# Optimization experiments

Measured on AMD Instinct MI355X. Metric: run time of the kernel, lower is better.

Reference implementation:

```python
import jax, jax.numpy as jnp
import numpy as np

B, N, D, H = 4, 2048, 64, 8

def setup_inputs() -> dict:
    key = jax.random.key(0)
    ks = jax.random.split(key, 6)
    s = 0.05
    return {
        "x":  jax.random.normal(ks[0], (B, N, D), dtype=jnp.float32),
        "Wq": jax.random.normal(ks[1], (D, D * H), dtype=jnp.float32) * s,
        "Wk": jax.random.normal(ks[2], (D, D * H), dtype=jnp.float32) * s,
        "Wv": jax.random.normal(ks[3], (D, D * H), dtype=jnp.float32) * s,
        "Wu": jax.random.normal(ks[4], (D * H, D), dtype=jnp.float32) * s,
        "bu": jnp.zeros((D,), dtype=jnp.float32),
    }

def reference(x, Wq, Wk, Wv, Wu, bu):
    b, n, d = x.shape
    h = Wq.shape[1] // d
    # projections: each head has full width d (per the original module)
    q = (x @ Wq).reshape(b, n, h, d).transpose(0, 2, 1, 3)  # [b,h,n,d]
    k = (x @ Wk).reshape(b, n, h, d).transpose(0, 2, 1, 3)
    v = (x @ Wv).reshape(b, n, h, d).transpose(0, 2, 1, 3)
    scores = jnp.einsum('bhnd,bhmd->bhnm', q, k) / jnp.sqrt(jnp.float32(d))
    w = jax.nn.softmax(scores, axis=-1)
    y = jnp.einsum('bhnm,bhmd->bhnd', w, v)          # [b,h,n,d]
    y = y.transpose(0, 2, 1, 3).reshape(b, n, h * d)  # [b,n,h*d]
    return y @ Wu + bu
```

## Files before the change

kernel.cpp:

```cpp
#include <hip/hip_runtime.h>
#include <hip/hip_bf16.h>

#define BB 4
#define NN 2048
#define DD 64
#define HH 8
#define DHH 512

typedef __bf16 bf16_t;
typedef __bf16 bf16x8 __attribute__((ext_vector_type(8)));
typedef __bf16 bf16x4 __attribute__((ext_vector_type(4)));
typedef float f32x4 __attribute__((ext_vector_type(4)));
typedef long long i64;
typedef i64 i64x2 __attribute__((ext_vector_type(2)));

__device__ __forceinline__ void dma16(const void* g, void* l) {
    __builtin_amdgcn_global_load_lds(
        (const __attribute__((address_space(1))) unsigned int*)g,
        (__attribute__((address_space(3))) unsigned int*)l,
        16, 0, 0);
}

#define MFMA __builtin_amdgcn_mfma_f32_16x16x32_bf16
#define MFMA8 __builtin_amdgcn_mfma_f32_16x16x32_fp8_fp8

#define QSCALE 0.18033688011112042f


__global__ __launch_bounds__(256) void prep(
    const float* __restrict__ Wq, const float* __restrict__ Wk,
    const float* __restrict__ Wv, const float* __restrict__ Wu,
    bf16_t* __restrict__ Wqt, bf16_t* __restrict__ Wkt,
    bf16_t* __restrict__ Wvt, bf16_t* __restrict__ Wut)
{
    const int bid = blockIdx.x, tid = threadIdx.x;
    if (bid < 12) {
        const int m = bid >> 2, slice = bid & 3;
        const float* src = (m == 0) ? Wq : (m == 1) ? Wk : Wv;
        bf16_t* dst = (m == 0) ? Wqt : (m == 1) ? Wkt : Wvt;
        const float scale = (m == 0) ? QSCALE : 1.0f;
        const int dc = slice * 128 + (tid >> 1);
        const int kbase = (tid & 1) * 32;
        #pragma unroll
        for (int k0 = 0; k0 < 4; ++k0) {
            bf16x8 p;
            #pragma unroll
            for (int j = 0; j < 8; ++j)
                p[j] = (bf16_t)(src[(size_t)(kbase + k0 * 8 + j) * 512 + dc] * scale);
            *(bf16x8*)(dst + dc * 64 + kbase + k0 * 8) = p;
        }
    } else {
        const int kq = (bid - 12) * 128;
        const int dc = tid >> 2, sub = (tid & 3) * 32;
        #pragma unroll
        for (int k0 = 0; k0 < 4; ++k0) {
            bf16x8 p;
            #pragma unroll
            for (int j = 0; j < 8; ++j)
                p[j] = (bf16_t)Wu[(size_t)(kq + sub + k0 * 8 + j) * 64 + dc];
            *(bf16x8*)(Wut + dc * 512 + kq + sub + k0 * 8) = p;
        }
    }
}

__global__ __launch_bounds__(256) void qkv_mfma(
    const float* __restrict__ x, const bf16_t* __restrict__ Wqt,
    const bf16_t* __restrict__ Wkt, const bf16_t* __restrict__ Wvt,
    char* __restrict__ q8, char* __restrict__ k8, bf16_t* __restrict__ vt)
{
    const int n0   = blockIdx.x * 64;
    const int h    = blockIdx.y;
    const int tid  = threadIdx.x;
    const int w    = tid >> 6;
    const int lane = tid & 63;
    const int quad = lane >> 4;
    const int c    = lane & 15;
    const int cq   = c & 7;
    const int l8   = lane >> 3;
    const int lg   = (lane & 7) ^ l8;
    const int lo   = l8 * 128 + lg * 16;
    const int sw0  = ((quad    ) ^ cq) * 16;
    const int sw1  = ((quad + 4) ^ cq) * 16;
    const int w2048 = w * 2048;

    __shared__ __align__(16) float  xs[64 * 64];
    __shared__ __align__(16) bf16_t Wqs[64 * 64], Wks[64 * 64], Wvs[64 * 64];

    {
        const int rloc = lane >> 4;
        const int s    = lane & 15;
        #pragma unroll
        for (int j = 0; j < 4; ++j) {
            int chunk = w * 4 + j;
            int r7 = (chunk * 4 + rloc) & 7;
            const char* src = (const char*)(x + (size_t)(n0 + chunk * 4 + rloc) * 64)
                            + ((s & 8) | ((s & 7) ^ r7)) * 16;
            dma16(src, (char*)xs + chunk * 1024);
        }
    }
    const char* qg = (const char*)Wqt + (size_t)h * 8192;
    const char* kg = (const char*)Wkt + (size_t)h * 8192;
    const char* vg = (const char*)Wvt + (size_t)h * 8192;
    dma16(qg + w2048 + lo,        (char*)Wqs + w2048);
    dma16(qg + w2048 + 1024 + lo, (char*)Wqs + w2048 + 1024);
    dma16(kg + w2048 + lo,        (char*)Wks + w2048);
    dma16(kg + w2048 + 1024 + lo, (char*)Wks + w2048 + 1024);
    dma16(vg + w2048 + lo,        (char*)Wvs + w2048);
    dma16(vg + w2048 + 1024 + lo, (char*)Wvs + w2048 + 1024);
    __syncthreads();

    auto xfrag = [&](int row, int kk) -> bf16x8 {
        const char* rbase = (const char*)xs + row * 256;
        int g0 = kk * 8 + ((quad * 2    ) ^ cq);
        int g1 = kk * 8 + ((quad * 2 + 1) ^ cq);
        f32x4 a = *(const f32x4*)(rbase + g0 * 16);
        f32x4 b = *(const f32x4*)(rbase + g1 * 16);
        bf16x8 r;
        r[0] = (bf16_t)a[0]; r[1] = (bf16_t)a[1]; r[2] = (bf16_t)a[2]; r[3] = (bf16_t)a[3];
        r[4] = (bf16_t)b[0]; r[5] = (bf16_t)b[1]; r[6] = (bf16_t)b[2]; r[7] = (bf16_t)b[3];
        return r;
    };

    bf16x8 xf0 = xfrag(w * 16 + c, 0);
    bf16x8 xf1 = xfrag(w * 16 + c, 1);

    const int gr = n0 + w * 16 + c;
    const int bb = gr >> 11, nn = gr & 2047;
    char* qrow_g = q8 + (((size_t)bb * HH + h) * NN + nn) * 64;
    char* krow_g = k8 + (((size_t)bb * HH + h) * NN + nn) * 64;
    const int nsw = nn & 3;

    #pragma unroll
    for (int mb = 0; mb < 4; ++mb) {
        const char* aq = (const char*)Wqs + (mb * 16 + c) * 128;
        const char* ak = (const char*)Wks + (mb * 16 + c) * 128;
        f32x4 accq = (f32x4){0.f, 0.f, 0.f, 0.f};
        f32x4 acck = (f32x4){0.f, 0.f, 0.f, 0.f};
        accq = MFMA(*(const bf16x8*)(aq + sw0), xf0, accq, 0, 0, 0);
        accq = MFMA(*(const bf16x8*)(aq + sw1), xf1, accq, 0, 0, 0);
        acck = MFMA(*(const bf16x8*)(ak + sw0), xf0, acck, 0, 0, 0);
        acck = MFMA(*(const bf16x8*)(ak + sw1), xf1, acck, 0, 0, 0);
        int g2  = (mb * 2 + (quad >> 1)) & 3;
        int off = ((quad & 1) * 4) + ((mb >> 1) * 8) + ((g2 ^ nsw) * 16);
        int pq = __builtin_amdgcn_cvt_pk_fp8_f32(accq[0], accq[1], 0, false);
        pq     = __builtin_amdgcn_cvt_pk_fp8_f32(accq[2], accq[3], pq, true);
        int pk = __builtin_amdgcn_cvt_pk_fp8_f32(acck[0], acck[1], 0, false);
        pk     = __builtin_amdgcn_cvt_pk_fp8_f32(acck[2], acck[3], pk, true);
        *(int*)(qrow_g + off) = pq;
        *(int*)(krow_g + off) = pk;
    }

    const char* wvrow = (const char*)Wvs + (w * 16 + c) * 128;
    bf16x8 vf0 = *(const bf16x8*)(wvrow + sw0);
    bf16x8 vf1 = *(const bf16x8*)(wvrow + sw1);

    const int bb2 = n0 >> 11;
    bf16_t* vtrow_g = vt + (((size_t)bb2 * HH + h) * DD + (w * 16 + c)) * NN + (n0 & 2047);

    #pragma unroll
    for (int nb = 0; nb < 4; ++nb) {
        f32x4 acc = (f32x4){0.f, 0.f, 0.f, 0.f};
        acc = MFMA(xfrag(nb * 16 + c, 0), vf0, acc, 0, 0, 0);
        acc = MFMA(xfrag(nb * 16 + c, 1), vf1, acc, 0, 0, 0);
        bf16x4 p = { (bf16_t)acc[0], (bf16_t)acc[1], (bf16_t)acc[2], (bf16_t)acc[3] };
        *(bf16x4*)(vtrow_g + nb * 16 + quad * 4) = p;
    }
}

__global__ __launch_bounds__(256, 4) void flash_attn(
    const char* __restrict__ q8, const char* __restrict__ k8,
    const bf16_t* __restrict__ vt, bf16_t* __restrict__ y)
{
    const int h    = blockIdx.x;
    const int n0   = blockIdx.y * 64;
    const int b    = blockIdx.z;
    const int tid  = threadIdx.x;
    const int w    = tid >> 6;
    const int lane = tid & 63;
    const int quad = lane >> 4;
    const int c    = lane & 15;
    const int cq   = c & 7;
    const int l8   = lane >> 3;
    const int lg   = (lane & 7) ^ l8;

    const int lo_v = l8 * 4096 + lg * 16;
    const int ksw  = (quad ^ (c & 3)) * 16;

    const int sw0 = ((quad    ) ^ cq) * 16;
    const int sw1 = ((quad + 4) ^ cq) * 16;
    int pw[4];
    #pragma unroll
    for (int nb = 0; nb < 4; ++nb)
        pw[nb] = (((nb * 2 + (quad >> 1)) ^ cq) * 16) + (quad & 1) * 8;
    const int crow = c * 128;
    const int prow = (w * 16 + c) * 128;

    __shared__ __align__(16) bf16_t Ps[64 * 64];
    __shared__ __align__(16) char   Ks[2][4096];
    __shared__ __align__(16) bf16_t Vs[2][64 * 64];

    const size_t bh = (size_t)(b * HH + h);
    const char* qp = q8 + bh * (size_t)(NN * 64);
    const char* kp = k8 + bh * (size_t)(NN * 64);
    const char* vp = (const char*)(vt + bh * (size_t)(DD * NN));

    i64x2 qf = *(const i64x2*)(qp + (size_t)(n0 + w * 16 + c) * 64 + ksw);

    const char* kptr  = kp + w * 1024 + lane * 16;
    const char* vptr  = vp + w * 65536 + lo_v;
    const char* vptr2 = vptr + 32768;

    dma16(kptr,  (char*)Ks[0] + w * 1024);
    dma16(vptr,  (char*)Vs[0] + w * 2048);
    dma16(vptr2, (char*)Vs[0] + w * 2048 + 1024);
    kptr += 4096; vptr += 128; vptr2 += 128;

    float lsum = 0.f;
    f32x4 o[4];
    #pragma unroll
    for (int db = 0; db < 4; ++db) o[db] = (f32x4){0.f, 0.f, 0.f, 0.f};

    __syncthreads();

    dma16(kptr,  (char*)Ks[1] + w * 1024);
    dma16(vptr,  (char*)Vs[1] + w * 2048);
    dma16(vptr2, (char*)Vs[1] + w * 2048 + 1024);
    kptr += 4096; vptr += 128; vptr2 += 128;

    char* pb = (char*)Ps;

    for (int kt = 0; kt < 32; ++kt) {
        const int buf = kt & 1;
        if (kt > 0) {
            __syncthreads();
            if (kt < 31) {
                dma16(kptr,  (char*)Ks[buf ^ 1] + w * 1024);
                dma16(vptr,  (char*)Vs[buf ^ 1] + w * 2048);
                dma16(vptr2, (char*)Vs[buf ^ 1] + w * 2048 + 1024);
                kptr += 4096; vptr += 128; vptr2 += 128;
            }
        }
        const char* kb = (const char*)Ks[buf];
        const char* vb = (const char*)Vs[buf];

        f32x4 s[4];
        #pragma unroll
        for (int nb = 0; nb < 4; ++nb) {
            i64x2 av = *(const i64x2*)(kb + (nb * 16 + c) * 64 + ksw);
            f32x4 t = (f32x4){0.f, 0.f, 0.f, 0.f};
            t = MFMA8(av.x, qf.x, t, 0, 0, 0);
            t = MFMA8(av.y, qf.y, t, 0, 0, 0);
            s[nb] = t;
        }

        #pragma unroll
        for (int nb = 0; nb < 4; ++nb) {
            float p0 = __builtin_amdgcn_exp2f(s[nb][0]);
            float p1 = __builtin_amdgcn_exp2f(s[nb][1]);
            float p2 = __builtin_amdgcn_exp2f(s[nb][2]);
            float p3 = __builtin_amdgcn_exp2f(s[nb][3]);
            lsum += (p0 + p1) + (p2 + p3);
            bf16x4 pk = { (bf16_t)p0, (bf16_t)p1, (bf16_t)p2, (bf16_t)p3 };
            *(bf16x4*)(pb + prow + pw[nb]) = pk;
        }

        bf16x8 pf0 = *(const bf16x8*)(pb + prow + sw0);
        bf16x8 pf1 = *(const bf16x8*)(pb + prow + sw1);

        #pragma unroll
        for (int db = 0; db < 4; ++db) {
            bf16x8 av0 = *(const bf16x8*)(vb + crow + db * 2048 + sw0);
            bf16x8 av1 = *(const bf16x8*)(vb + crow + db * 2048 + sw1);
            o[db] = MFMA(av0, pf0, o[db], 0, 0, 0);
            o[db] = MFMA(av1, pf1, o[db], 0, 0, 0);
        }
    }

    float l = lsum;
    l += __shfl_xor(l, 16, 64);
    l += __shfl_xor(l, 32, 64);
    float inv = 1.0f / l;

    #pragma unroll
    for (int db = 0; db < 4; ++db) {
        bf16x4 pk = { (bf16_t)(o[db][0] * inv), (bf16_t)(o[db][1] * inv),
                      (bf16_t)(o[db][2] * inv), (bf16_t)(o[db][3] * inv) };
        *(bf16x4*)(pb + prow + pw[db]) = pk;
    }
    __syncthreads();

    bf16_t* ypb = y + bh * (size_t)(NN * DD) + (size_t)n0 * DD;
    #pragma unroll
    for (int it = 0; it < 2; ++it) {
        int idx  = it * 256 + tid;
        int row  = idx >> 3;
        int gpos = idx & 7;
        int g    = gpos ^ (row & 7);
        bf16x8 val = *(const bf16x8*)((const char*)Ps + idx * 16);
        *(bf16x8*)(ypb + (size_t)row * DD + g * 8) = val;
    }
}

__global__ __launch_bounds__(256) void out_proj(
    const bf16_t* __restrict__ y,
    const bf16_t* __restrict__ Wut,
    const float* __restrict__ bu, float* __restrict__ out)
{
    const int rt   = blockIdx.x >> 1;
    const int dh   = blockIdx.x & 1;
    const int row0 = rt * 32;
    const int b    = row0 >> 11;
    const int nn0  = row0 & 2047;
    const int tid  = threadIdx.x;
    const int w    = tid >> 6;
    const int lane = tid & 63;
    const int quad = lane >> 4;
    const int c    = lane & 15;
    const int cq   = c & 7;

    __shared__ __align__(16) bf16_t ys[32 * 512];

    {
        const int hsel = lane >> 3;
        const int g7   = lane & 7;
        #pragma unroll
        for (int rr = 0; rr < 8; ++rr) {
            int row = w * 8 + rr;
            const char* src = (const char*)y
                + (((size_t)b * HH + hsel) * NN + nn0 + row) * 128
                + ((g7 ^ (row & 7)) * 16);
            dma16(src, (char*)ys + row * 1024);
        }
    }
    __syncthreads();

    const int rows16 = (w >> 1) * 16;
    const int mb     = dh * 2 + (w & 1);
    const char* yrow = (const char*)ys + (rows16 + c) * 1024;

    f32x4 acc = (f32x4){0.f, 0.f, 0.f, 0.f};
    #pragma unroll
    for (int kk = 0; kk < 16; ++kk) {
        int g = kk * 4 + quad;
        bf16x8 bfrag = *(const bf16x8*)(yrow + (((g & ~7) | ((g & 7) ^ cq)) * 16));
        bf16x8 afrag = *(const bf16x8*)((const char*)Wut
                        + (size_t)(mb * 16 + c) * 1024 + kk * 64 + quad * 16);
        acc = MFMA(afrag, bfrag, acc, 0, 0, 0);
    }

    float4 bb = *(const float4*)(bu + mb * 16 + quad * 4);
    float4 res = { acc[0] + bb.x, acc[1] + bb.y, acc[2] + bb.z, acc[3] + bb.w };
    float* op = out + (size_t)(row0 + rows16 + c) * DD + mb * 16 + quad * 4;
    *(float4*)op = res;
}

extern "C" void kernel_launch(void* const* d_in, const int* in_sizes, int n_in,
                              void* d_out, int out_size, void* d_ws, size_t ws_size,
                              hipStream_t stream) {
    const float* x  = (const float*)d_in[0];
    const float* Wq = (const float*)d_in[1];
    const float* Wk = (const float*)d_in[2];
    const float* Wv = (const float*)d_in[3];
    const float* Wu = (const float*)d_in[4];
    const float* bu = (const float*)d_in[5];
    float* out = (float*)d_out;

    const size_t SEG8 = (size_t)BB * HH * NN * 64;
    const size_t SEG  = SEG8 * 2;
    char* ws = (char*)d_ws;
    char*   q8  = ws;
    char*   k8  = ws + SEG8;
    bf16_t* vt  = (bf16_t*)(ws + 2 * SEG8);
    bf16_t* y   = (bf16_t*)(ws + 2 * SEG8 + SEG);
    bf16_t* Wqt = (bf16_t*)(ws + 2 * SEG8 + 2 * SEG);
    bf16_t* Wkt = (bf16_t*)(ws + 2 * SEG8 + 2 * SEG + (1 << 16));
    bf16_t* Wvt = (bf16_t*)(ws + 2 * SEG8 + 2 * SEG + 2 * (1 << 16));
    bf16_t* Wut = (bf16_t*)(ws + 2 * SEG8 + 2 * SEG + 3 * (1 << 16));

    prep<<<dim3(16), dim3(256), 0, stream>>>(Wq, Wk, Wv, Wu, Wqt, Wkt, Wvt, Wut);
    qkv_mfma<<<dim3(128, 8), dim3(256), 0, stream>>>(x, Wqt, Wkt, Wvt, q8, k8, vt);
    flash_attn<<<dim3(HH, NN / 64, BB), dim3(256), 0, stream>>>(q8, k8, vt, y);
    out_proj<<<dim3(512), dim3(256), 0, stream>>>(y, Wut, bu, out);
}
```

Baseline: 133.5 us.

## Restructure flash attention to split keys across waves with register-resident P

```diff
diff --git a/kernel.cpp b/kernel.cpp
--- a/kernel.cpp
+++ b/kernel.cpp
@@ -13,6 +13,9 @@
 typedef float f32x4 __attribute__((ext_vector_type(4)));
 typedef long long i64;
 typedef i64 i64x2 __attribute__((ext_vector_type(2)));
+typedef _Float16 f16_t;
+typedef _Float16 f16x4 __attribute__((ext_vector_type(4)));
+typedef __fp16 h16x2 __attribute__((ext_vector_type(2)));
 
 __device__ __forceinline__ void dma16(const void* g, void* l) {
     __builtin_amdgcn_global_load_lds(
@@ -21,8 +24,9 @@
         16, 0, 0);
 }
 
-#define MFMA __builtin_amdgcn_mfma_f32_16x16x32_bf16
-#define MFMA8 __builtin_amdgcn_mfma_f32_16x16x32_fp8_fp8
+#define MFMA   __builtin_amdgcn_mfma_f32_16x16x32_bf16
+#define MFMA8  __builtin_amdgcn_mfma_f32_16x16x32_fp8_fp8
+#define MFMA16F __builtin_amdgcn_mfma_f32_16x16x16f16
 
 #define QSCALE 0.18033688011112042f
 
@@ -66,7 +70,7 @@
 __global__ __launch_bounds__(256) void qkv_mfma(
     const float* __restrict__ x, const bf16_t* __restrict__ Wqt,
     const bf16_t* __restrict__ Wkt, const bf16_t* __restrict__ Wvt,
-    char* __restrict__ q8, char* __restrict__ k8, bf16_t* __restrict__ vt)
+    char* __restrict__ q8, char* __restrict__ k8, f16_t* __restrict__ vt)
 {
     const int n0   = blockIdx.x * 64;
     const int h    = blockIdx.y;
@@ -155,21 +159,21 @@
     bf16x8 vf1 = *(const bf16x8*)(wvrow + sw1);
 
     const int bb2 = n0 >> 11;
-    bf16_t* vtrow_g = vt + (((size_t)bb2 * HH + h) * DD + (w * 16 + c)) * NN + (n0 & 2047);
+    f16_t* vtrow_g = vt + (((size_t)bb2 * HH + h) * DD + (w * 16 + c)) * NN + (n0 & 2047);
 
     #pragma unroll
     for (int nb = 0; nb < 4; ++nb) {
         f32x4 acc = (f32x4){0.f, 0.f, 0.f, 0.f};
         acc = MFMA(xfrag(nb * 16 + c, 0), vf0, acc, 0, 0, 0);
         acc = MFMA(xfrag(nb * 16 + c, 1), vf1, acc, 0, 0, 0);
-        bf16x4 p = { (bf16_t)acc[0], (bf16_t)acc[1], (bf16_t)acc[2], (bf16_t)acc[3] };
-        *(bf16x4*)(vtrow_g + nb * 16 + quad * 4) = p;
+        f16x4 p = { (f16_t)acc[0], (f16_t)acc[1], (f16_t)acc[2], (f16_t)acc[3] };
+        *(f16x4*)(vtrow_g + nb * 16 + quad * 4) = p;
     }
 }
 
 __global__ __launch_bounds__(256, 4) void flash_attn(
     const char* __restrict__ q8, const char* __restrict__ k8,
-    const bf16_t* __restrict__ vt, bf16_t* __restrict__ y)
+    const f16_t* __restrict__ vt, bf16_t* __restrict__ y)
 {
     const int h    = blockIdx.x;
     const int n0   = blockIdx.y * 64;
@@ -179,125 +183,123 @@
     const int lane = tid & 63;
     const int quad = lane >> 4;
     const int c    = lane & 15;
-    const int cq   = c & 7;
-    const int l8   = lane >> 3;
-    const int lg   = (lane & 7) ^ l8;
-
-    const int lo_v = l8 * 4096 + lg * 16;
     const int ksw  = (quad ^ (c & 3)) * 16;
 
-    const int sw0 = ((quad    ) ^ cq) * 16;
-    const int sw1 = ((quad + 4) ^ cq) * 16;
-    int pw[4];
-    #pragma unroll
-    for (int nb = 0; nb < 4; ++nb)
-        pw[nb] = (((nb * 2 + (quad >> 1)) ^ cq) * 16) + (quad & 1) * 8;
-    const int crow = c * 128;
-    const int prow = (w * 16 + c) * 128;
-
-    __shared__ __align__(16) bf16_t Ps[64 * 64];
-    __shared__ __align__(16) char   Ks[2][4096];
-    __shared__ __align__(16) bf16_t Vs[2][64 * 64];
+    __shared__ __align__(16) char LB[17408];
 
     const size_t bh = (size_t)(b * HH + h);
     const char* qp = q8 + bh * (size_t)(NN * 64);
     const char* kp = k8 + bh * (size_t)(NN * 64);
     const char* vp = (const char*)(vt + bh * (size_t)(DD * NN));
 
-    i64x2 qf = *(const i64x2*)(qp + (size_t)(n0 + w * 16 + c) * 64 + ksw);
-
-    const char* kptr  = kp + w * 1024 + lane * 16;
-    const char* vptr  = vp + w * 65536 + lo_v;
-    const char* vptr2 = vptr + 32768;
-
-    dma16(kptr,  (char*)Ks[0] + w * 1024);
-    dma16(vptr,  (char*)Vs[0] + w * 2048);
-    dma16(vptr2, (char*)Vs[0] + w * 2048 + 1024);
-    kptr += 4096; vptr += 128; vptr2 += 128;
-
-    float lsum = 0.f;
-    f32x4 o[4];
-    #pragma unroll
-    for (int db = 0; db < 4; ++db) o[db] = (f32x4){0.f, 0.f, 0.f, 0.f};
-
-    __syncthreads();
-
-    dma16(kptr,  (char*)Ks[1] + w * 1024);
-    dma16(vptr,  (char*)Vs[1] + w * 2048);
-    dma16(vptr2, (char*)Vs[1] + w * 2048 + 1024);
-    kptr += 4096; vptr += 128; vptr2 += 128;
-
-    char* pb = (char*)Ps;
+    i64x2 qf[4];
+    #pragma unroll
+    for (int cb = 0; cb < 4; ++cb)
+        qf[cb] = *(const i64x2*)(qp + (size_t)(n0 + cb * 16 + c) * 64 + ksw);
+
+    const char* kfp = kp + (size_t)(w * 16 + c) * 64 + ksw;
+    const char* vfp = vp + (size_t)c * 4096 + w * 32 + quad * 8;
+
+    i64x2 kf = *(const i64x2*)(kfp);
+    f16x4 vf[4];
+    #pragma unroll
+    for (int db = 0; db < 4; ++db)
+        vf[db] = *(const f16x4*)(vfp + db * 65536);
+
+    float lsum[4] = {0.f, 0.f, 0.f, 0.f};
+    f32x4 o[4][4];
+    #pragma unroll
+    for (int db = 0; db < 4; ++db)
+        #pragma unroll
+        for (int cb = 0; cb < 4; ++cb) o[db][cb] = (f32x4){0.f, 0.f, 0.f, 0.f};
 
     for (int kt = 0; kt < 32; ++kt) {
-        const int buf = kt & 1;
-        if (kt > 0) {
-            __syncthreads();
-            if (kt < 31) {
-                dma16(kptr,  (char*)Ks[buf ^ 1] + w * 1024);
-                dma16(vptr,  (char*)Vs[buf ^ 1] + w * 2048);
-                dma16(vptr2, (char*)Vs[buf ^ 1] + w * 2048 + 1024);
-                kptr += 4096; vptr += 128; vptr2 += 128;
+        const int kt2 = (kt + 1) & 31;
+        i64x2 kf_n = *(const i64x2*)(kfp + (size_t)kt2 * 4096);
+        f16x4 vf_n[4];
+        #pragma unroll
+        for (int db = 0; db < 4; ++db)
+            vf_n[db] = *(const f16x4*)(vfp + db * 65536 + (size_t)kt2 * 128);
+
+        #pragma unroll
+        for (int cb = 0; cb < 4; ++cb) {
+            f32x4 s = (f32x4){0.f, 0.f, 0.f, 0.f};
+            s = MFMA8(kf.x, qf[cb].x, s, 0, 0, 0);
+            s = MFMA8(kf.y, qf[cb].y, s, 0, 0, 0);
+            float p0 = __builtin_amdgcn_exp2f(s[0]);
+            float p1 = __builtin_amdgcn_exp2f(s[1]);
+            float p2 = __builtin_amdgcn_exp2f(s[2]);
+            float p3 = __builtin_amdgcn_exp2f(s[3]);
+            lsum[cb] += (p0 + p1) + (p2 + p3);
+            h16x2 ab = __builtin_amdgcn_cvt_pkrtz(p0, p1);
+            h16x2 cd = __builtin_amdgcn_cvt_pkrtz(p2, p3);
+            f16x4 pf = { (f16_t)ab[0], (f16_t)ab[1], (f16_t)cd[0], (f16_t)cd[1] };
+            #pragma unroll
+            for (int db = 0; db < 4; ++db)
+                o[db][cb] = MFMA16F(vf[db], pf, o[db][cb], 0, 0, 0);
+        }
+
+        kf = kf_n;
+        #pragma unroll
+        for (int db = 0; db < 4; ++db) vf[db] = vf_n[db];
+    }
+
+    char* Ob = LB;
+    float* Lb = (float*)(LB + 16384);
+
+    #pragma unroll
+    for (int cb = 0; cb < 4; ++cb) {
+        lsum[cb] += __shfl_xor(lsum[cb], 16, 64);
+        lsum[cb] += __shfl_xor(lsum[cb], 32, 64);
+    }
+    if (quad == 0) {
+        #pragma unroll
+        for (int cb = 0; cb < 4; ++cb)
+            Lb[(w * 4 + cb) * 16 + c] = lsum[cb];
+    }
+
+    #pragma unroll
+    for (int ww = 0; ww < 4; ++ww) {
+        if (w == ww) {
+            #pragma unroll
+            for (int db = 0; db < 4; ++db) {
+                #pragma unroll
+                for (int cb = 0; cb < 4; ++cb) {
+                    char* p = Ob + (size_t)(((db * 4 + cb) * 4 + quad) * 16 + c) * 16;
+                    f32x4 v = o[db][cb];
+                    if (ww > 0) v += *(const f32x4*)p;
+                    *(f32x4*)p = v;
+                }
             }
         }
-        const char* kb = (const char*)Ks[buf];
-        const char* vb = (const char*)Vs[buf];
-
-        f32x4 s[4];
-        #pragma unroll
-        for (int nb = 0; nb < 4; ++nb) {
-            i64x2 av = *(const i64x2*)(kb + (nb * 16 + c) * 64 + ksw);
-            f32x4 t = (f32x4){0.f, 0.f, 0.f, 0.f};
-            t = MFMA8(av.x, qf.x, t, 0, 0, 0);
-            t = MFMA8(av.y, qf.y, t, 0, 0, 0);
-            s[nb] = t;
-        }
-
-        #pragma unroll
-        for (int nb = 0; nb < 4; ++nb) {
-            float p0 = __builtin_amdgcn_exp2f(s[nb][0]);
-            float p1 = __builtin_amdgcn_exp2f(s[nb][1]);
-            float p2 = __builtin_amdgcn_exp2f(s[nb][2]);
-            float p3 = __builtin_amdgcn_exp2f(s[nb][3]);
-            lsum += (p0 + p1) + (p2 + p3);
-            bf16x4 pk = { (bf16_t)p0, (bf16_t)p1, (bf16_t)p2, (bf16_t)p3 };
-            *(bf16x4*)(pb + prow + pw[nb]) = pk;
-        }
-
-        bf16x8 pf0 = *(const bf16x8*)(pb + prow + sw0);
-        bf16x8 pf1 = *(const bf16x8*)(pb + prow + sw1);
-
-        #pragma unroll
-        for (int db = 0; db < 4; ++db) {
-            bf16x8 av0 = *(const bf16x8*)(vb + crow + db * 2048 + sw0);
-            bf16x8 av1 = *(const bf16x8*)(vb + crow + db * 2048 + sw1);
-            o[db] = MFMA(av0, pf0, o[db], 0, 0, 0);
-            o[db] = MFMA(av1, pf1, o[db], 0, 0, 0);
-        }
-    }
-
-    float l = lsum;
-    l += __shfl_xor(l, 16, 64);
-    l += __shfl_xor(l, 32, 64);
-    float inv = 1.0f / l;
-
-    #pragma unroll
-    for (int db = 0; db < 4; ++db) {
-        bf16x4 pk = { (bf16_t)(o[db][0] * inv), (bf16_t)(o[db][1] * inv),
-                      (bf16_t)(o[db][2] * inv), (bf16_t)(o[db][3] * inv) };
-        *(bf16x4*)(pb + prow + pw[db]) = pk;
-    }
-    __syncthreads();
-
-    bf16_t* ypb = y + bh * (size_t)(NN * DD) + (size_t)n0 * DD;
-    #pragma unroll
-    for (int it = 0; it < 2; ++it) {
-        int idx  = it * 256 + tid;
-        int row  = idx >> 3;
-        int gpos = idx & 7;
-        int g    = gpos ^ (row & 7);
-        bf16x8 val = *(const bf16x8*)((const char*)Ps + idx * 16);
-        *(bf16x8*)(ypb + (size_t)row * DD + g * 8) = val;
+        __syncthreads();
+    }
+
+    {
+        const int n_loc = tid & 63;
+        const int dq    = tid >> 6;
+        const int qcb   = n_loc >> 4;
+        const int cc    = n_loc & 15;
+        float l = Lb[(0 * 4 + qcb) * 16 + cc] + Lb[(1 * 4 + qcb) * 16 + cc]
+                + Lb[(2 * 4 + qcb) * 16 + cc] + Lb[(3 * 4 + qcb) * 16 + cc];
+        float inv = 1.0f / l;
+        float vals[16];
+        #pragma unroll
+        for (int q2 = 0; q2 < 4; ++q2) {
+            f32x4 v = *(const f32x4*)(Ob
+                    + (size_t)(((dq * 4 + qcb) * 4 + q2) * 16 + cc) * 16);
+            vals[q2 * 4 + 0] = v[0]; vals[q2 * 4 + 1] = v[1];
+            vals[q2 * 4 + 2] = v[2]; vals[q2 * 4 + 3] = v[3];
+        }
+        bf16x8 o0, o1;
+        #pragma unroll
+        for (int j = 0; j < 8; ++j) {
+            o0[j] = (bf16_t)(vals[j] * inv);
+            o1[j] = (bf16_t)(vals[8 + j] * inv);
+        }
+        bf16_t* yrow = y + bh * (size_t)(NN * DD) + (size_t)(n0 + n_loc) * DD + dq * 16;
+        *(bf16x8*)(yrow)     = o0;
+        *(bf16x8*)(yrow + 8) = o1;
     }
 }
 
@@ -370,7 +372,7 @@
     char* ws = (char*)d_ws;
     char*   q8  = ws;
     char*   k8  = ws + SEG8;
-    bf16_t* vt  = (bf16_t*)(ws + 2 * SEG8);
+    f16_t*  vt  = (f16_t*)(ws + 2 * SEG8);
     bf16_t* y   = (bf16_t*)(ws + 2 * SEG8 + SEG);
     bf16_t* Wqt = (bf16_t*)(ws + 2 * SEG8 + 2 * SEG);
     bf16_t* Wkt = (bf16_t*)(ws + 2 * SEG8 + 2 * SEG + (1 << 16));
```

Measured after the change: 156.2 us. 17.0% more time.
